# Kernel optimization log

Measured on AMD Instinct MI355X. Metric: run time of the kernel, lower is better.

Reference implementation:

```python
import jax, jax.numpy as jnp
import numpy as np

NUM_HEADS = 16


def setup_inputs() -> dict:
    key = jax.random.key(0)
    k1, k2, k3 = jax.random.split(key, 3)
    T, B, E = 2048, 2, 1024
    query = jax.random.normal(k1, (T, B, E), dtype=jnp.float32)
    # xavier-uniform-ish init for qkv weight, small normal for output proj
    lim = (6.0 / (3 * E + E)) ** 0.5
    W_qkv = jax.random.uniform(k2, (3 * E, E), dtype=jnp.float32, minval=-lim, maxval=lim)
    W_o = jax.random.normal(k3, (E, E), dtype=jnp.float32) * 0.02
    b_qkv = jnp.zeros((3 * E,), dtype=jnp.float32)
    b_o = jnp.zeros((E,), dtype=jnp.float32)
    return {"query": query, "W_qkv": W_qkv, "b_qkv": b_qkv, "W_o": W_o, "b_o": b_o}


def reference(query, W_qkv, b_qkv, W_o, b_o):
    T, B, E = query.shape
    H = NUM_HEADS
    hd = E // H
    scaling = float(hd) ** -0.5

    # fused qkv projection: [T, B, 3E]
    qkv = jnp.einsum('tbe,fe->tbf', query, W_qkv) + b_qkv
    q, k, v = jnp.split(qkv, 3, axis=-1)
    q = q * scaling

    def to_heads(x):  # [T, B, E] -> [B*H, T, hd]
        return x.reshape(T, B * H, hd).transpose(1, 0, 2)

    q, k, v = to_heads(q), to_heads(k), to_heads(v)

    # explicit bmm QK^T -> softmax -> bmm AV (faithful to source)
    scores = jnp.einsum('bqd,bkd->bqk', q, k)          # [B*H, T, T]
    attn = jax.nn.softmax(scores, axis=-1)             # dropout p=0.0 (eval)
    ctx = jnp.einsum('bqk,bkd->bqd', attn, v)          # [B*H, T, hd]

    out = ctx.transpose(1, 0, 2).reshape(T, B, E)
    out = jnp.einsum('tbe,fe->tbf', out, W_o) + b_o    # o_net

    avg_weights = attn.reshape(B, H, T, T).sum(axis=1) / H  # need_weights=True path
    return out, avg_weights
```

## Files before the change

kernel.cpp:

```cpp
#include <hip/hip_runtime.h>
#include <stdint.h>

typedef unsigned short u16;
typedef __bf16 bf16x8 __attribute__((ext_vector_type(8)));
typedef float f32x4 __attribute__((ext_vector_type(4)));
typedef float f32x16 __attribute__((ext_vector_type(16)));

__device__ __forceinline__ u16 f2b(float f) {
  unsigned u = __builtin_bit_cast(unsigned, f);
  u += 0x7fffu + ((u >> 16) & 1u);
  return (u16)(u >> 16);
}

__device__ __forceinline__ float fexp2(float x) { return __builtin_amdgcn_exp2f(x); }

__device__ __forceinline__ void gld_lds16(const void* g, void* l) {
  __builtin_amdgcn_global_load_lds((const __attribute__((address_space(1))) unsigned int*)g,
                                   (__attribute__((address_space(3))) unsigned int*)l,
                                   16, 0, 0);
}

__global__ __launch_bounds__(256) void k_cvt3(
    const float* __restrict__ s0, u16* __restrict__ d0,
    const float* __restrict__ s1, u16* __restrict__ d1,
    const float* __restrict__ s2, u16* __restrict__ d2) {
  const int bx = blockIdx.x;
  const float* s;
  u16* d;
  int i0;
  if (bx < 4096)      { s = s0; d = d0; i0 = bx; }
  else if (bx < 7168) { s = s1; d = d1; i0 = bx - 4096; }
  else                { s = s2; d = d2; i0 = bx - 7168; }
  const int i = i0 * 256 + threadIdx.x;
  float4 v = reinterpret_cast<const float4*>(s)[i];
  ushort4 o;
  o.x = f2b(v.x); o.y = f2b(v.y); o.z = f2b(v.z); o.w = f2b(v.w);
  reinterpret_cast<ushort4*>(d)[i] = o;
}

template <int EPI>
__device__ __forceinline__ void gemm_body(
    const u16* __restrict__ A, const u16* __restrict__ B, const float* __restrict__ bias,
    float* __restrict__ outF, u16* __restrict__ q_ws, u16* __restrict__ k_ws,
    u16* __restrict__ vt_ws, int tm, int tn, u16* smem) {
  u16* Al0 = smem;
  u16* Bl0 = smem + 8192;
  const int tid = threadIdx.x;
  const int w = tid >> 6, lane = tid & 63;
  const int wr = w >> 1, wc = w & 1;
  const int lo = lane & 15, hi = lane >> 4;
  const size_t arow0 = (size_t)tm * 128;
  const size_t brow0 = (size_t)tn * 128;

  f32x4 acc[4][4] = {};

  const int rr = lane >> 2;
  const int kswz = ((lane & 3) ^ ((rr >> 1) & 3)) * 8;
  const int rsw = (lo >> 1) & 3;

  for (int rs = 0; rs < 2; ++rs) {
    int seg = rs * 4 + w;
    gld_lds16(A + (arow0 + seg * 16 + rr) * 1024 + kswz, &Al0[seg * 512 + lane * 8]);
    gld_lds16(B + (brow0 + seg * 16 + rr) * 1024 + kswz, &Bl0[seg * 512 + lane * 8]);
  }
  __syncthreads();
  int cur = 0;
  for (int kb = 0; kb < 32; ++kb) {
    if (kb + 1 < 32) {
      const int k0 = (kb + 1) * 32 + kswz;
      u16* Ad = Al0 + (cur ^ 1) * 4096;
      u16* Bd = Bl0 + (cur ^ 1) * 4096;
      for (int rs = 0; rs < 2; ++rs) {
        int seg = rs * 4 + w;
        gld_lds16(A + (arow0 + seg * 16 + rr) * 1024 + k0, &Ad[seg * 512 + lane * 8]);
        gld_lds16(B + (brow0 + seg * 16 + rr) * 1024 + k0, &Bd[seg * 512 + lane * 8]);
      }
    }
    const u16* Ac = Al0 + cur * 4096;
    const u16* Bc = Bl0 + cur * 4096;
    bf16x8 af[4], bfr[4];
#pragma unroll
    for (int m = 0; m < 4; ++m)
      af[m] = *(const bf16x8*)&Ac[(wr * 64 + m * 16 + lo) * 32 + ((hi ^ rsw) * 8)];
#pragma unroll
    for (int n = 0; n < 4; ++n)
      bfr[n] = *(const bf16x8*)&Bc[(wc * 64 + n * 16 + lo) * 32 + ((hi ^ rsw) * 8)];
#pragma unroll
    for (int m = 0; m < 4; ++m)
#pragma unroll
      for (int n = 0; n < 4; ++n)
        acc[m][n] = __builtin_amdgcn_mfma_f32_16x16x32_bf16(af[m], bfr[n], acc[m][n], 0, 0, 0);
    __syncthreads();
    cur ^= 1;
  }

  if (EPI == 0) {
#pragma unroll
    for (int n = 0; n < 4; ++n) {
      const int col = tn * 128 + wc * 64 + n * 16 + lo;
      const float bb = bias[col];
#pragma unroll
      for (int m = 0; m < 4; ++m)
#pragma unroll
        for (int r = 0; r < 4; ++r) {
          const int row = tm * 128 + wr * 64 + m * 16 + hi * 4 + r;
          outF[(size_t)row * 1024 + col] = acc[m][n][r] + bb;
        }
    }
  } else {
    const int sec = tn >> 3;
#pragma unroll
    for (int n = 0; n < 4; ++n) {
      const int cin = (tn & 7) * 128 + wc * 64 + n * 16 + lo;
      const int h = cin >> 6, d = cin & 63;
      const float bb = bias[sec * 1024 + cin];
#pragma unroll
      for (int m = 0; m < 4; ++m) {
        const int rowb = tm * 128 + wr * 64 + m * 16 + hi * 4;
        const int t0 = rowb >> 1;
        const float v0 = acc[m][n][0] + bb, v1 = acc[m][n][1] + bb;
        const float v2 = acc[m][n][2] + bb, v3 = acc[m][n][3] + bb;
        if (sec == 0) {
          const float s = 0.18033688f;
          q_ws[(((size_t)h * 2048 + t0) * 64) + d]            = f2b(v0 * s);
          q_ws[(((size_t)(16 + h) * 2048 + t0) * 64) + d]     = f2b(v1 * s);
          q_ws[(((size_t)h * 2048 + t0 + 1) * 64) + d]        = f2b(v2 * s);
          q_ws[(((size_t)(16 + h) * 2048 + t0 + 1) * 64) + d] = f2b(v3 * s);
        } else if (sec == 1) {
          k_ws[(((size_t)h * 2048 + t0) * 64) + d]            = f2b(v0);
          k_ws[(((size_t)(16 + h) * 2048 + t0) * 64) + d]     = f2b(v1);
          k_ws[(((size_t)h * 2048 + t0 + 1) * 64) + d]        = f2b(v2);
          k_ws[(((size_t)(16 + h) * 2048 + t0 + 1) * 64) + d] = f2b(v3);
        } else {
          const int tp0 = (t0 & ~12) | ((t0 & 4) << 1) | ((t0 & 8) >> 1);
          ushort2 p0, p1;
          p0.x = f2b(v0); p0.y = f2b(v2);
          p1.x = f2b(v1); p1.y = f2b(v3);
          *(ushort2*)(vt_ws + ((size_t)h * 64 + d) * 2048 + tp0) = p0;
          *(ushort2*)(vt_ws + ((size_t)(16 + h) * 64 + d) * 2048 + tp0) = p1;
        }
      }
    }
  }
}

__global__ __launch_bounds__(256) void k_gemm_qkv(
    const u16* __restrict__ A, const u16* __restrict__ B, const float* __restrict__ bias,
    u16* __restrict__ q_ws, u16* __restrict__ k_ws, u16* __restrict__ vt_ws) {
  __shared__ __align__(16) u16 smem[16384];
  const int flat = blockIdx.y * 24 + blockIdx.x;
  const int xcd = flat & 7, idx = flat >> 3;
  const int wg = xcd * 96 + idx;
  gemm_body<1>(A, B, bias, nullptr, q_ws, k_ws, vt_ws, wg / 24, wg % 24, smem);
}

__device__ __forceinline__ void avg_body(
    const u16* __restrict__ q_ws, const u16* __restrict__ k_ws,
    const float* __restrict__ c_ws, float* __restrict__ avg,
    int kx, int qy, int b, u16* smem) {
  u16* Kl0 = smem;
  const int tid = threadIdx.x, w = tid >> 6, lane = tid & 63;
  const int lo = lane & 15, hi = lane >> 4;
  const int kbase = kx * 128;
  const int qb = qy * 64;
  const int qrow = qb + w * 16 + lo;
  const int qrow_base = qb + w * 16 + hi * 4;
  const int l7 = lo & 7;

  const int r0 = tid >> 3, c0 = tid & 7;
  const int xc = (c0 ^ (r0 & 7)) * 8;
  const u16* kg = k_ws + ((size_t)(b * 16) * 2048 + kbase + r0) * 64 + xc;

  float acc[8][4] = {};
  const f32x4 zero = {0.f, 0.f, 0.f, 0.f};

#pragma unroll
  for (int j = 0; j < 4; ++j)
    gld_lds16(kg + j * 32 * 64, Kl0 + (tid + 256 * j) * 8);
  __syncthreads();

  int cur = 0;
  for (int h = 0; h < 16; ++h) {
    const int bh = b * 16 + h;
    if (h + 1 < 16) {
      const u16* kgn = kg + (size_t)(h + 1) * 2048 * 64;
      u16* dst = Kl0 + (cur ^ 1) * 8192;
#pragma unroll
      for (int j = 0; j < 4; ++j)
        gld_lds16(kgn + j * 32 * 64, dst + (tid + 256 * j) * 8);
    }
    const u16* qp = q_ws + ((size_t)bh * 2048 + qrow) * 64 + hi * 8;
    bf16x8 qf0 = *(const bf16x8*)qp;
    bf16x8 qf1 = *(const bf16x8*)(qp + 32);
    const float4 cf = *(const float4*)(c_ws + (size_t)bh * 2048 + qrow_base);
    const float cfa[4] = {cf.x, cf.y, cf.z, cf.w};
    const char* kbse = (const char*)(Kl0 + cur * 8192);
#pragma unroll
    for (int n = 0; n < 8; ++n) {
      const char* kp = kbse + (n * 16 + lo) * 128;
      bf16x8 k0 = *(const bf16x8*)(kp + ((hi ^ l7) << 4));
      bf16x8 k1 = *(const bf16x8*)(kp + (((hi + 4) ^ l7) << 4));
      f32x4 s = __builtin_amdgcn_mfma_f32_16x16x32_bf16(qf0, k0, zero, 0, 0, 0);
      s = __builtin_amdgcn_mfma_f32_16x16x32_bf16(qf1, k1, s, 0, 0, 0);
#pragma unroll
      for (int r = 0; r < 4; ++r) acc[n][r] += fexp2(s[r]) * cfa[r];
    }
    __syncthreads();
    cur ^= 1;
  }

  const float s16 = 1.0f / 16.0f;
#pragma unroll
  for (int n = 0; n < 8; ++n)
#pragma unroll
    for (int r = 0; r < 4; ++r)
      avg[((size_t)(b * 2048 + qrow_base + r)) * 2048 + kbase + n * 16 + lo] = acc[n][r] * s16;
}

__global__ __launch_bounds__(256) void k_tail(
    const u16* __restrict__ ctx, const u16* __restrict__ wobf, const float* __restrict__ bo,
    float* __restrict__ out, const u16* __restrict__ q_ws, const u16* __restrict__ k_ws,
    const float* __restrict__ c_ws, float* __restrict__ avg) {
  __shared__ __align__(16) u16 smem[16384];
  const int bx = blockIdx.x;
  if (bx < 256) {
    gemm_body<0>(ctx, wobf, bo, out, nullptr, nullptr, nullptr, bx >> 3, bx & 7, smem);
  } else {
    const int id = bx - 256;
    avg_body(q_ws, k_ws, c_ws, avg, id & 15, (id >> 4) & 31, id >> 9, smem);
  }
}

__global__ __launch_bounds__(1024) void k_flash(
    const u16* __restrict__ q_ws, const u16* __restrict__ k_ws, const u16* __restrict__ vt_ws,
    u16* __restrict__ ctx_ws, float* __restrict__ c_ws) {
  __shared__ __align__(16) u16 KVl[33792];
  const int tid = threadIdx.x, w = tid >> 6, lane = tid & 63;
  const int h = lane >> 5, l31 = lane & 31, l7 = lane & 7;
  const int hh = w >> 3;
  const int wq = w & 7;
  const int tid_h = tid & 511;

  const int flat = blockIdx.y * 8 + blockIdx.x;
  const int xcd = flat & 7, idx = flat >> 3;
  const int bh = xcd * 4 + (idx & 3);
  const int qtile = idx >> 2;
  const int b = bh >> 4, head = bh & 15;
  const int qbase = qtile * 256;
  const int qrow = qbase + wq * 32 + l31;

  bf16x8 qf[4];
#pragma unroll
  for (int j = 0; j < 4; ++j)
    qf[j] = *(const bf16x8*)(q_ws + ((size_t)bh * 2048 + qrow) * 64 + j * 16 + h * 8);

  const int srow = tid_h >> 3, schk = tid_h & 7;
  const int xc = (schk ^ (srow & 7)) * 8;
  const u16* kgA = k_ws + ((size_t)bh * 2048 + hh * 1024 + srow) * 64 + xc;
  const u16* vgA = vt_ws + ((size_t)bh * 64 + srow) * 2048 + hh * 1024 + xc;

  f32x16 ca0 = {}, ca1 = {};
  float lrow = 0.f;

  {
    u16* base = KVl + hh * 8192;
    gld_lds16(kgA, base + tid_h * 8);
    gld_lds16(vgA, base + 4096 + tid_h * 8);
  }
  __syncthreads();

  int cur = 0;
  for (int it = 0; it < 16; ++it) {
    if (it < 15) {
      u16* base = KVl + (cur ^ 1) * 16384 + hh * 8192;
      gld_lds16(kgA + (size_t)(it + 1) * 4096, base + tid_h * 8);
      gld_lds16(vgA + (it + 1) * 64, base + 4096 + tid_h * 8);
    }
    const char* Kb = (const char*)(KVl + cur * 16384 + hh * 8192);
    const char* Vb = Kb + 8192;

    f32x16 st0 = {}, st1 = {};
    __builtin_amdgcn_s_setprio(1);
#pragma unroll
    for (int j = 0; j < 4; ++j) {
      bf16x8 k0 = *(const bf16x8*)(Kb + l31 * 128 + (((2 * j + h) ^ l7) * 16));
      bf16x8 k1 = *(const bf16x8*)(Kb + (32 + l31) * 128 + (((2 * j + h) ^ l7) * 16));
      st0 = __builtin_amdgcn_mfma_f32_32x32x16_bf16(k0, qf[j], st0, 0, 0, 0);
      st1 = __builtin_amdgcn_mfma_f32_32x32x16_bf16(k1, qf[j], st1, 0, 0, 0);
    }
    __builtin_amdgcn_s_setprio(0);

    float ps0 = 0.f, ps1 = 0.f;
#pragma unroll
    for (int r = 0; r < 16; ++r) { float p = fexp2(st0[r]); st0[r] = p; ps0 += p; }
#pragma unroll
    for (int r = 0; r < 16; ++r) { float p = fexp2(st1[r]); st1[r] = p; ps1 += p; }
    float ps = ps0 + ps1;
    ps += __shfl_xor(ps, 32, 64);
    lrow += ps;

    bf16x8 pb00, pb01, pb10, pb11;
#pragma unroll
    for (int i = 0; i < 8; ++i) {
      pb00[i] = (__bf16)st0[i];
      pb01[i] = (__bf16)st0[8 + i];
      pb10[i] = (__bf16)st1[i];
      pb11[i] = (__bf16)st1[8 + i];
    }

    __builtin_amdgcn_s_setprio(1);
#pragma unroll
    for (int t2 = 0; t2 < 2; ++t2)
#pragma unroll
      for (int kp = 0; kp < 2; ++kp) {
        const int ch = (4 * t2 + 2 * kp + h) ^ l7;
        bf16x8 v0 = *(const bf16x8*)(Vb + l31 * 128 + ch * 16);
        bf16x8 v1 = *(const bf16x8*)(Vb + (32 + l31) * 128 + ch * 16);
        const bf16x8 pv = (t2 == 0) ? (kp == 0 ? pb00 : pb01) : (kp == 0 ? pb10 : pb11);
        ca0 = __builtin_amdgcn_mfma_f32_32x32x16_bf16(v0, pv, ca0, 0, 0, 0);
        ca1 = __builtin_amdgcn_mfma_f32_32x32x16_bf16(v1, pv, ca1, 0, 0, 0);
      }
    __builtin_amdgcn_s_setprio(0);

    __syncthreads();
    cur ^= 1;
  }

  float* F = (float*)KVl;
  if (w >= 8) {
    const int g = w - 8;
#pragma unroll
    for (int r = 0; r < 16; ++r) {
      F[g * 2048 + r * 64 + lane] = ca0[r];
      F[g * 2048 + (16 + r) * 64 + lane] = ca1[r];
    }
    F[16384 + g * 64 + lane] = lrow;
  }
  __syncthreads();
  float inv = 0.f;
  if (w < 8) {
#pragma unroll
    for (int r = 0; r < 16; ++r) {
      ca0[r] += F[w * 2048 + r * 64 + lane];
      ca1[r] += F[w * 2048 + (16 + r) * 64 + lane];
    }
    lrow += F[16384 + w * 64 + lane];
    inv = 1.0f / lrow;
    if (lane < 32) c_ws[(size_t)bh * 2048 + qrow] = inv;
  }
  __syncthreads();
  u16* tw = KVl + w * 2048;
  if (w < 8) {
#pragma unroll
    for (int r = 0; r < 16; ++r) {
      const int d0 = (r & 3) + 8 * (r >> 2) + 4 * h;
      const int d1 = 32 + d0;
      *(u16*)((char*)tw + l31 * 128 + ((2 * d0) ^ (l7 << 4))) = f2b(ca0[r] * inv);
      *(u16*)((char*)tw + l31 * 128 + ((2 * d1) ^ (l7 << 4))) = f2b(ca1[r] * inv);
    }
  }
  __syncthreads();
  if (w < 8) {
#pragma unroll
    for (int it = 0; it < 4; ++it) {
      const int row = it * 8 + (lane >> 3);
      uint4 val = *(const uint4*)((const char*)tw + row * 128 + (((lane & 7) ^ (row & 7)) * 16));
      const int q = qbase + wq * 32 + row;
      *(uint4*)(ctx_ws + ((size_t)(q * 2 + b)) * 1024 + head * 64 + (lane & 7) * 8) = val;
    }
  }
}

extern "C" void kernel_launch(void* const* d_in, const int* in_sizes, int n_in,
                              void* d_out, int out_size, void* d_ws, size_t ws_size,
                              hipStream_t stream) {
  const float* query = (const float*)d_in[0];
  const float* Wqkv  = (const float*)d_in[1];
  const float* bqkv  = (const float*)d_in[2];
  const float* Wo    = (const float*)d_in[3];
  const float* bo    = (const float*)d_in[4];
  float* out = (float*)d_out;
  float* avg = out + (size_t)4096 * 1024;

  char* ws = (char*)d_ws;
  u16* qbf    = (u16*)(ws);
  u16* ctx_ws = (u16*)(ws);
  u16*   wqkvbf = (u16*)(ws + 8388608);
  float* c_ws   = (float*)(ws + 8388608);
  u16* wobf  = (u16*)(ws + 14680064);
  u16* q_ws  = (u16*)(ws + 16777216);
  u16* k_ws  = (u16*)(ws + 25165824);
  u16* vt_ws = (u16*)(ws + 33554432);

  k_cvt3<<<dim3(8192), dim3(256), 0, stream>>>(query, qbf, Wqkv, wqkvbf, Wo, wobf);
  k_gemm_qkv<<<dim3(24, 32), dim3(256), 0, stream>>>(
      qbf, wqkvbf, bqkv, q_ws, k_ws, vt_ws);
  k_flash<<<dim3(8, 32), dim3(1024), 0, stream>>>(
      q_ws, k_ws, vt_ws, ctx_ws, c_ws);
  k_tail<<<dim3(1280), dim3(256), 0, stream>>>(
      ctx_ws, wobf, bo, out, q_ws, k_ws, c_ws, avg);
}
```

Measured before the change: 139.9 us.

## Write K in MFMA fragment layout so avg-weights path skips LDS staging

The QKV GEMM epilogue now also writes a second copy of K in a layout pre-arranged for the MFMA B-operand, so each lane can load its fragment directly from global memory. The averaged-attention-weights kernel then reads K straight from that buffer instead of staging it through LDS with double buffering and barriers. This removes the LDS traffic and synchronisation from the avg path, at the cost of extra scattered 2-byte stores in the GEMM epilogue and an extra workspace buffer. A fallback keeps the old path when the workspace is too small.

```diff
diff --git a/kernel.cpp b/kernel.cpp
--- a/kernel.cpp
+++ b/kernel.cpp
@@ -38,11 +38,11 @@
   reinterpret_cast<ushort4*>(d)[i] = o;
 }
 
-template <int EPI>
+template <int EPI, int K2>
 __device__ __forceinline__ void gemm_body(
     const u16* __restrict__ A, const u16* __restrict__ B, const float* __restrict__ bias,
     float* __restrict__ outF, u16* __restrict__ q_ws, u16* __restrict__ k_ws,
-    u16* __restrict__ vt_ws, int tm, int tn, u16* smem) {
+    u16* __restrict__ vt_ws, u16* __restrict__ k2, int tm, int tn, u16* smem) {
   u16* Al0 = smem;
   u16* Bl0 = smem + 8192;
   const int tid = threadIdx.x;
@@ -127,10 +127,19 @@
           q_ws[(((size_t)h * 2048 + t0 + 1) * 64) + d]        = f2b(v2 * s);
           q_ws[(((size_t)(16 + h) * 2048 + t0 + 1) * 64) + d] = f2b(v3 * s);
         } else if (sec == 1) {
-          k_ws[(((size_t)h * 2048 + t0) * 64) + d]            = f2b(v0);
-          k_ws[(((size_t)(16 + h) * 2048 + t0) * 64) + d]     = f2b(v1);
-          k_ws[(((size_t)h * 2048 + t0 + 1) * 64) + d]        = f2b(v2);
-          k_ws[(((size_t)(16 + h) * 2048 + t0 + 1) * 64) + d] = f2b(v3);
+          const u16 b0 = f2b(v0), b1 = f2b(v1), b2 = f2b(v2), b3 = f2b(v3);
+          k_ws[(((size_t)h * 2048 + t0) * 64) + d]            = b0;
+          k_ws[(((size_t)(16 + h) * 2048 + t0) * 64) + d]     = b1;
+          k_ws[(((size_t)h * 2048 + t0 + 1) * 64) + d]        = b2;
+          k_ws[(((size_t)(16 + h) * 2048 + t0 + 1) * 64) + d] = b3;
+          if (K2) {
+            const int kb2 = t0 >> 7, nn = (t0 >> 4) & 7, lo2 = t0 & 15;
+            const size_t base = ((size_t)kb2 * 8 + nn) * 1024 + ((d >> 3) * 16 + lo2) * 8 + (d & 7);
+            k2[(size_t)h * 131072 + base]            = b0;
+            k2[(size_t)h * 131072 + base + 8]        = b2;
+            k2[(size_t)(16 + h) * 131072 + base]     = b1;
+            k2[(size_t)(16 + h) * 131072 + base + 8] = b3;
+          }
         } else {
           const int tp0 = (t0 & ~12) | ((t0 & 4) << 1) | ((t0 & 8) >> 1);
           ushort2 p0, p1;
@@ -144,17 +153,19 @@
   }
 }
 
+template <int K2>
 __global__ __launch_bounds__(256) void k_gemm_qkv(
     const u16* __restrict__ A, const u16* __restrict__ B, const float* __restrict__ bias,
-    u16* __restrict__ q_ws, u16* __restrict__ k_ws, u16* __restrict__ vt_ws) {
+    u16* __restrict__ q_ws, u16* __restrict__ k_ws, u16* __restrict__ vt_ws,
+    u16* __restrict__ k2) {
   __shared__ __align__(16) u16 smem[16384];
   const int flat = blockIdx.y * 24 + blockIdx.x;
   const int xcd = flat & 7, idx = flat >> 3;
   const int wg = xcd * 96 + idx;
-  gemm_body<1>(A, B, bias, nullptr, q_ws, k_ws, vt_ws, wg / 24, wg % 24, smem);
-}
-
-__device__ __forceinline__ void avg_body(
+  gemm_body<1, K2>(A, B, bias, nullptr, q_ws, k_ws, vt_ws, k2, wg / 24, wg % 24, smem);
+}
+
+__device__ __forceinline__ void avg_body_lds(
     const u16* __restrict__ q_ws, const u16* __restrict__ k_ws,
     const float* __restrict__ c_ws, float* __restrict__ avg,
     int kx, int qy, int b, u16* smem) {
@@ -217,17 +228,63 @@
       avg[((size_t)(b * 2048 + qrow_base + r)) * 2048 + kbase + n * 16 + lo] = acc[n][r] * s16;
 }
 
+__device__ __forceinline__ void avg_body_k2(
+    const u16* __restrict__ q_ws, const u16* __restrict__ k2,
+    const float* __restrict__ c_ws, float* __restrict__ avg,
+    int kx, int qy, int b) {
+  const int tid = threadIdx.x, w = tid >> 6, lane = tid & 63;
+  const int lo = lane & 15, hi = lane >> 4;
+  const int kbase = kx * 128;
+  const int qb = qy * 64;
+  const int qrow = qb + w * 16 + lo;
+  const int qrow_base = qb + w * 16 + hi * 4;
+
+  float acc[8][4] = {};
+  const f32x4 zero = {0.f, 0.f, 0.f, 0.f};
+
+  for (int h = 0; h < 16; ++h) {
+    const int bh = b * 16 + h;
+    const u16* qp = q_ws + ((size_t)bh * 2048 + qrow) * 64 + hi * 8;
+    bf16x8 qf0 = *(const bf16x8*)qp;
+    bf16x8 qf1 = *(const bf16x8*)(qp + 32);
+    const float4 cf = *(const float4*)(c_ws + (size_t)bh * 2048 + qrow_base);
+    const float cfa[4] = {cf.x, cf.y, cf.z, cf.w};
+    const u16* kp2 = k2 + ((size_t)bh * 16 + kx) * 8192 + lane * 8;
+#pragma unroll
+    for (int n = 0; n < 8; ++n) {
+      bf16x8 k0 = *(const bf16x8*)(kp2 + n * 1024);
+      bf16x8 k1 = *(const bf16x8*)(kp2 + n * 1024 + 512);
+      f32x4 s = __builtin_amdgcn_mfma_f32_16x16x32_bf16(qf0, k0, zero, 0, 0, 0);
+      s = __builtin_amdgcn_mfma_f32_16x16x32_bf16(qf1, k1, s, 0, 0, 0);
+#pragma unroll
+      for (int r = 0; r < 4; ++r) acc[n][r] += fexp2(s[r]) * cfa[r];
+    }
+  }
+
+  const float s16 = 1.0f / 16.0f;
+#pragma unroll
+  for (int n = 0; n < 8; ++n)
+#pragma unroll
+    for (int r = 0; r < 4; ++r)
+      avg[((size_t)(b * 2048 + qrow_base + r)) * 2048 + kbase + n * 16 + lo] = acc[n][r] * s16;
+}
+
+template <int PATH>
 __global__ __launch_bounds__(256) void k_tail(
     const u16* __restrict__ ctx, const u16* __restrict__ wobf, const float* __restrict__ bo,
     float* __restrict__ out, const u16* __restrict__ q_ws, const u16* __restrict__ k_ws,
-    const float* __restrict__ c_ws, float* __restrict__ avg) {
+    const u16* __restrict__ k2, const float* __restrict__ c_ws, float* __restrict__ avg) {
   __shared__ __align__(16) u16 smem[16384];
   const int bx = blockIdx.x;
   if (bx < 256) {
-    gemm_body<0>(ctx, wobf, bo, out, nullptr, nullptr, nullptr, bx >> 3, bx & 7, smem);
+    gemm_body<0, 0>(ctx, wobf, bo, out, nullptr, nullptr, nullptr, nullptr,
+                    bx >> 3, bx & 7, smem);
   } else {
     const int id = bx - 256;
-    avg_body(q_ws, k_ws, c_ws, avg, id & 15, (id >> 4) & 31, id >> 9, smem);
+    if (PATH)
+      avg_body_k2(q_ws, k2, c_ws, avg, id & 15, (id >> 4) & 31, id >> 9);
+    else
+      avg_body_lds(q_ws, k_ws, c_ws, avg, id & 15, (id >> 4) & 31, id >> 9, smem);
   }
 }
 
@@ -391,12 +448,25 @@
   u16* q_ws  = (u16*)(ws + 16777216);
   u16* k_ws  = (u16*)(ws + 25165824);
   u16* vt_ws = (u16*)(ws + 33554432);
+  u16* k2_ws = (u16*)(ws + 41943040);
+
+  const bool k2ok = ws_size >= 50331648ull;
 
   k_cvt3<<<dim3(8192), dim3(256), 0, stream>>>(query, qbf, Wqkv, wqkvbf, Wo, wobf);
-  k_gemm_qkv<<<dim3(24, 32), dim3(256), 0, stream>>>(
-      qbf, wqkvbf, bqkv, q_ws, k_ws, vt_ws);
+  if (k2ok) {
+    k_gemm_qkv<1><<<dim3(24, 32), dim3(256), 0, stream>>>(
+        qbf, wqkvbf, bqkv, q_ws, k_ws, vt_ws, k2_ws);
+  } else {
+    k_gemm_qkv<0><<<dim3(24, 32), dim3(256), 0, stream>>>(
+        qbf, wqkvbf, bqkv, q_ws, k_ws, vt_ws, nullptr);
+  }
   k_flash<<<dim3(8, 32), dim3(1024), 0, stream>>>(
       q_ws, k_ws, vt_ws, ctx_ws, c_ws);
-  k_tail<<<dim3(1280), dim3(256), 0, stream>>>(
-      ctx_ws, wobf, bo, out, q_ws, k_ws, c_ws, avg);
-}
+  if (k2ok) {
+    k_tail<1><<<dim3(1280), dim3(256), 0, stream>>>(
+        ctx_ws, wobf, bo, out, q_ws, k_ws, k2_ws, c_ws, avg);
+  } else {
+    k_tail<0><<<dim3(1280), dim3(256), 0, stream>>>(
+        ctx_ws, wobf, bo, out, q_ws, k_ws, nullptr, c_ws, avg);
+  }
+}
```

Measured after the change: 178.5 us. +27.6%, slower.
